# Kernel tuning notes

Hardware: AMD Instinct MI355X
Metric: run time of the kernel (lower is better)

Reference implementation:

```python
import jax, jax.numpy as jnp
import numpy as np

B, Q, K, D, H = 16, 128, 128, 512, 512
NEG = -1e6


def setup_inputs() -> dict:
    key = jax.random.key(0)
    ks = jax.random.split(key, 7)
    return {
        "queries": jax.random.normal(ks[0], (B, Q, D), dtype=jnp.float32),
        "keys": jax.random.normal(ks[1], (B, K, D), dtype=jnp.float32),
        "values": jax.random.normal(ks[2], (B, K, D), dtype=jnp.float32),
        "valid_lens": jax.random.randint(ks[3], (B,), 1, K + 1, dtype=jnp.int32),
        "Wq": jax.random.normal(ks[4], (D, H), dtype=jnp.float32) / np.sqrt(D),
        "Wk": jax.random.normal(ks[5], (D, H), dtype=jnp.float32) / np.sqrt(D),
        "wv": jax.random.normal(ks[6], (H,), dtype=jnp.float32) / np.sqrt(H),
    }


def reference(queries, keys, values, valid_lens, Wq, Wk, wv):
    # projections (LazyLinear, bias=False)
    q = jnp.einsum("bqd,dh->bqh", queries, Wq)  # [B,Q,H]
    k = jnp.einsum("bkd,dh->bkh", keys, Wk)    # [B,K,H]
    # broadcast add -> tanh -> reduce to scalar score (Bahdanau)
    feats = jnp.tanh(q[:, :, None, :] + k[:, None, :, :])  # [B,Q,K,H]
    scores = jnp.einsum("bqkh,h->bqk", feats, wv)           # [B,Q,K]
    # masked softmax over key dim using per-batch valid lengths
    mask = jnp.arange(scores.shape[-1])[None, None, :] < valid_lens[:, None, None]
    scores = jnp.where(mask, scores, NEG)
    attn = jax.nn.softmax(scores, axis=-1)                  # [B,Q,K]
    # dropout is identity in eval mode
    return jnp.einsum("bqk,bkv->bqv", attn, values)
```

## Files before the change

### kernel.cpp

```cpp
#include <hip/hip_runtime.h>

#define Bn 16
#define Qn 128
#define Kn 128
#define Dn 512
#define Hn 512
#define NEGV (-3.0e38f)
#define PSCALE 2.8853900817779268f

typedef short s16x8 __attribute__((ext_vector_type(8)));
typedef float f32x4 __attribute__((ext_vector_type(4)));

__device__ __forceinline__ float exp2_hw(float x) {
  float r;
  asm("v_exp_f32 %0, %1" : "=v"(r) : "v"(x));
  return r;
}
__device__ __forceinline__ float rcp_hw(float x) { return __builtin_amdgcn_rcpf(x); }
__device__ __forceinline__ unsigned short f2bf(float f) {
  unsigned int u = __float_as_uint(f);
  u += 0x7fff + ((u >> 16) & 1);
  return (unsigned short)(u >> 16);
}

__global__ __launch_bounds__(256) void convert_kernel(
    const float* __restrict__ queries, const float* __restrict__ keys,
    const float* __restrict__ Wq, const float* __restrict__ Wk,
    const float* __restrict__ values,
    unsigned short* __restrict__ Abf, unsigned short* __restrict__ Wt,
    unsigned short* __restrict__ Vt)
{
  const int bid = blockIdx.x, t = threadIdx.x;
  if (bid < 512) {
    const int gid = bid * 256 + t;
    const size_t base = (size_t)gid * 16;
    const float* src = (base < 1048576) ? (queries + base) : (keys + (base - 1048576));
    unsigned short o[16];
    #pragma unroll
    for (int j = 0; j < 4; ++j) {
      float4 v = *(const float4*)(src + j * 4);
      o[j * 4 + 0] = f2bf(v.x); o[j * 4 + 1] = f2bf(v.y);
      o[j * 4 + 2] = f2bf(v.z); o[j * 4 + 3] = f2bf(v.w);
    }
    #pragma unroll
    for (int j = 0; j < 4; ++j)
      *(ushort4*)(Abf + base + j * 4) = *(ushort4*)&o[j * 4];
  } else if (bid < 640) {
    const int tid = (bid - 512) * 256 + t;
    const int n = tid & 511, rest = tid >> 9;
    const int sel = rest >> 5, k16 = rest & 31;
    const float* W = sel ? Wk : Wq;
    unsigned short o[16];
    #pragma unroll
    for (int i = 0; i < 16; ++i)
      o[i] = f2bf(W[(size_t)(k16 * 16 + i) * Hn + n]);
    unsigned short* dst = Wt + (size_t)sel * 262144 + (size_t)n * 512 + k16 * 16;
    #pragma unroll
    for (int j = 0; j < 4; ++j) *(ushort4*)(dst + j * 4) = *(ushort4*)&o[j * 4];
  } else {
    const int tid = (bid - 640) * 256 + t;
    const int d = tid & 511, rest = tid >> 9;
    const int b = rest >> 2, k32 = rest & 3;
    unsigned short o[32];
    #pragma unroll
    for (int i = 0; i < 32; ++i)
      o[i] = f2bf(values[((size_t)(b * Kn + k32 * 32 + i)) * Dn + d]);
    unsigned short* dst = Vt + (size_t)b * 65536 + (size_t)d * 128 + k32 * 32;
    #pragma unroll
    for (int j = 0; j < 8; ++j) *(ushort4*)(dst + j * 4) = *(ushort4*)&o[j * 4];
  }
}

__global__ __launch_bounds__(256) void proj_mfma(
    const unsigned short* __restrict__ Abf, const unsigned short* __restrict__ Wt,
    const float* __restrict__ wv,
    float* __restrict__ QW, float* __restrict__ Ekq)
{
  __shared__ unsigned short Al[128][72];
  __shared__ unsigned short Bl[64][72];
  const int t = threadIdx.x, w = t >> 6, l = t & 63;
  const int wm = w >> 1, wn = w & 1;
  const int rowTile = blockIdx.x;
  const int n0 = blockIdx.y * 64;
  const int R0 = rowTile * 128;
  const bool isQ = rowTile < 16;
  const unsigned short* Wsel = Wt + (isQ ? 0 : 262144);

  f32x4 acc[4][2];
  #pragma unroll
  for (int m = 0; m < 4; ++m)
    #pragma unroll
    for (int n = 0; n < 2; ++n) acc[m][n] = (f32x4)0.f;

  const int lr = l & 15, lk = l >> 4;

  for (int k0 = 0; k0 < Hn; k0 += 64) {
    ushort4 ar[4][2], br[2][2];
    #pragma unroll
    for (int i = 0; i < 4; ++i) {
      int g = t + 256 * i, r = g >> 3, c = g & 7;
      const unsigned short* p = Abf + (size_t)(R0 + r) * Hn + k0 + c * 8;
      ar[i][0] = *(const ushort4*)p; ar[i][1] = *(const ushort4*)(p + 4);
    }
    #pragma unroll
    for (int i = 0; i < 2; ++i) {
      int g = t + 256 * i, r = g >> 3, c = g & 7;
      const unsigned short* p = Wsel + (size_t)(n0 + r) * Hn + k0 + c * 8;
      br[i][0] = *(const ushort4*)p; br[i][1] = *(const ushort4*)(p + 4);
    }
    __syncthreads();
    #pragma unroll
    for (int i = 0; i < 4; ++i) {
      int g = t + 256 * i, r = g >> 3, c = g & 7;
      *(ushort4*)&Al[r][c * 8] = ar[i][0]; *(ushort4*)&Al[r][c * 8 + 4] = ar[i][1];
    }
    #pragma unroll
    for (int i = 0; i < 2; ++i) {
      int g = t + 256 * i, r = g >> 3, c = g & 7;
      *(ushort4*)&Bl[r][c * 8] = br[i][0]; *(ushort4*)&Bl[r][c * 8 + 4] = br[i][1];
    }
    __syncthreads();
    #pragma unroll
    for (int ks = 0; ks < 2; ++ks) {
      s16x8 af[4], bf_[2];
      #pragma unroll
      for (int m = 0; m < 4; ++m)
        af[m] = *(const s16x8*)&Al[wm * 64 + m * 16 + lr][ks * 32 + lk * 8];
      #pragma unroll
      for (int n = 0; n < 2; ++n)
        bf_[n] = *(const s16x8*)&Bl[wn * 32 + n * 16 + lr][ks * 32 + lk * 8];
      #pragma unroll
      for (int m = 0; m < 4; ++m)
        #pragma unroll
        for (int n = 0; n < 2; ++n)
          acc[m][n] = __builtin_amdgcn_mfma_f32_16x16x32_bf16(af[m], bf_[n], acc[m][n], 0, 0, 0);
    }
    __syncthreads();
  }

  #pragma unroll
  for (int m = 0; m < 4; ++m)
    #pragma unroll
    for (int n = 0; n < 2; ++n)
      #pragma unroll
      for (int r = 0; r < 4; ++r) {
        int row = R0 + wm * 64 + m * 16 + lk * 4 + r;
        int col = n0 + wn * 32 + n * 16 + lr;
        float a = acc[m][n][r];
        if (isQ) {
          float F  = exp2_hw(-PSCALE * a);
          float WF = -2.f * wv[col] * F;
          float2 o = {WF, F};
          *(float2*)(QW + ((size_t)row * Hn + col) * 2) = o;
        } else {
          int krow = row - 2048;
          int bb = krow >> 7, k = krow & 127;
          Ekq[(size_t)bb * 65536 + (size_t)col * 128 + k] = exp2_hw(PSCALE * a);
        }
      }
}

__global__ __launch_bounds__(256) void score_kernel(
    const float* __restrict__ QW, const float* __restrict__ Ekq,
    float* __restrict__ Sp)
{
  const int id = blockIdx.x;
  const int g = id & 63, qt = id >> 6;
  const int b = g >> 2, hs = g & 3;
  const int t = threadIdx.x, w = t >> 6, l = t & 63;
  const int q  = qt * 16 + w * 4 + (l >> 4);
  const int k0 = (l & 15) * 8;
  const int h0 = hs * 128;

  const float* ek  = Ekq + (size_t)b * 65536 + (size_t)h0 * 128 + k0;
  const float* qwp = QW + ((size_t)(b * Qn + q) * Hn + h0) * 2;

  float acc[8];
  #pragma unroll
  for (int j = 0; j < 8; ++j) acc[j] = 0.f;

  float4 e0a = *(const float4*)(ek);
  float4 e0b = *(const float4*)(ek + 4);
  float4 e1a = *(const float4*)(ek + 128);
  float4 e1b = *(const float4*)(ek + 132);
  float4 qv  = *(const float4*)(qwp);

  #pragma unroll 2
  for (int hb = 0; hb < 64; ++hb) {
    float4 ce0a = e0a, ce0b = e0b, ce1a = e1a, ce1b = e1b, cqv = qv;
    if (hb < 63) {
      const float* ep = ek + (size_t)(2 * hb + 2) * 128;
      e0a = *(const float4*)(ep);
      e0b = *(const float4*)(ep + 4);
      e1a = *(const float4*)(ep + 128);
      e1b = *(const float4*)(ep + 132);
      qv  = *(const float4*)(qwp + hb * 4 + 4);
    }
    const float WF0 = cqv.x, F0 = cqv.y, WF1 = cqv.z, F1 = cqv.w;
    float d0, d1, num;
    d0 = F0 + ce0a.x; d1 = F1 + ce1a.x;
    num = __builtin_fmaf(WF0, d1, WF1 * d0);
    acc[0] = __builtin_fmaf(num, rcp_hw(d0 * d1), acc[0]);
    d0 = F0 + ce0a.y; d1 = F1 + ce1a.y;
    num = __builtin_fmaf(WF0, d1, WF1 * d0);
    acc[1] = __builtin_fmaf(num, rcp_hw(d0 * d1), acc[1]);
    d0 = F0 + ce0a.z; d1 = F1 + ce1a.z;
    num = __builtin_fmaf(WF0, d1, WF1 * d0);
    acc[2] = __builtin_fmaf(num, rcp_hw(d0 * d1), acc[2]);
    d0 = F0 + ce0a.w; d1 = F1 + ce1a.w;
    num = __builtin_fmaf(WF0, d1, WF1 * d0);
    acc[3] = __builtin_fmaf(num, rcp_hw(d0 * d1), acc[3]);
    d0 = F0 + ce0b.x; d1 = F1 + ce1b.x;
    num = __builtin_fmaf(WF0, d1, WF1 * d0);
    acc[4] = __builtin_fmaf(num, rcp_hw(d0 * d1), acc[4]);
    d0 = F0 + ce0b.y; d1 = F1 + ce1b.y;
    num = __builtin_fmaf(WF0, d1, WF1 * d0);
    acc[5] = __builtin_fmaf(num, rcp_hw(d0 * d1), acc[5]);
    d0 = F0 + ce0b.z; d1 = F1 + ce1b.z;
    num = __builtin_fmaf(WF0, d1, WF1 * d0);
    acc[6] = __builtin_fmaf(num, rcp_hw(d0 * d1), acc[6]);
    d0 = F0 + ce0b.w; d1 = F1 + ce1b.w;
    num = __builtin_fmaf(WF0, d1, WF1 * d0);
    acc[7] = __builtin_fmaf(num, rcp_hw(d0 * d1), acc[7]);
  }

  float4 o0 = {acc[0], acc[1], acc[2], acc[3]};
  float4 o1 = {acc[4], acc[5], acc[6], acc[7]};
  size_t sb = (((size_t)hs * Bn + b) * Qn + q) * Kn + k0;
  *(float4*)(Sp + sb) = o0;
  *(float4*)(Sp + sb + 4) = o1;
}

__global__ __launch_bounds__(512) void softmax_kernel(
    const float* __restrict__ Sp, const int* __restrict__ valid_lens,
    unsigned short* __restrict__ At)
{
  const int t = threadIdx.x;
  const int b = blockIdx.y;
  const int q = blockIdx.x * 16 + (t >> 5);
  const int k0 = (t & 31) * 4;
  const size_t base = ((size_t)b * Qn + q) * Kn + k0;

  float4 s0 = *(const float4*)(Sp + base);
  float4 s1 = *(const float4*)(Sp + base + 262144);
  float4 s2 = *(const float4*)(Sp + base + 524288);
  float4 s3 = *(const float4*)(Sp + base + 786432);
  float s[4] = {s0.x + s1.x + s2.x + s3.x, s0.y + s1.y + s2.y + s3.y,
                s0.z + s1.z + s2.z + s3.z, s0.w + s1.w + s2.w + s3.w};

  const int vlen = valid_lens[b];
  bool ok[4];
  float m = NEGV;
  #pragma unroll
  for (int j = 0; j < 4; ++j) {
    ok[j] = (k0 + j) < vlen;
    if (ok[j]) m = fmaxf(m, s[j]);
  }
  #pragma unroll
  for (int xm = 16; xm >= 1; xm >>= 1) m = fmaxf(m, __shfl_xor(m, xm, 32));
  float e[4], sum = 0.f;
  #pragma unroll
  for (int j = 0; j < 4; ++j) {
    e[j] = ok[j] ? exp2_hw((s[j] - m) * 1.44269504f) : 0.f;
    sum += e[j];
  }
  #pragma unroll
  for (int xm = 16; xm >= 1; xm >>= 1) sum += __shfl_xor(sum, xm, 32);
  float inv = rcp_hw(sum);
  ushort4 o = {f2bf(e[0] * inv), f2bf(e[1] * inv), f2bf(e[2] * inv), f2bf(e[3] * inv)};
  *(ushort4*)(At + base) = o;
}

__global__ __launch_bounds__(256) void av_mfma(
    const unsigned short* __restrict__ At, const unsigned short* __restrict__ Vt,
    float* __restrict__ out)
{
  __shared__ unsigned short AtL[128][72];
  __shared__ unsigned short VL[128][72];
  const int t = threadIdx.x, w = t >> 6, l = t & 63;
  const int wm = w >> 1, wn = w & 1;
  const int dt = blockIdx.x;
  const int b = blockIdx.y;
  const int lr = l & 15, lk = l >> 4;

  f32x4 acc[4][4];
  #pragma unroll
  for (int m = 0; m < 4; ++m)
    #pragma unroll
    for (int n = 0; n < 4; ++n) acc[m][n] = (f32x4)0.f;

  const unsigned short* Atb = At + (size_t)b * Qn * Kn;
  const unsigned short* Vtb = Vt + (size_t)b * 65536 + (size_t)dt * 128 * Kn;

  for (int k0 = 0; k0 < Kn; k0 += 64) {
    ushort4 ar[4][2], vr[4][2];
    #pragma unroll
    for (int i = 0; i < 4; ++i) {
      int g = t + 256 * i, r = g >> 3, c = g & 7;
      const unsigned short* p = Atb + (size_t)r * Kn + k0 + c * 8;
      ar[i][0] = *(const ushort4*)p; ar[i][1] = *(const ushort4*)(p + 4);
      const unsigned short* pv = Vtb + (size_t)r * Kn + k0 + c * 8;
      vr[i][0] = *(const ushort4*)pv; vr[i][1] = *(const ushort4*)(pv + 4);
    }
    __syncthreads();
    #pragma unroll
    for (int i = 0; i < 4; ++i) {
      int g = t + 256 * i, r = g >> 3, c = g & 7;
      *(ushort4*)&AtL[r][c * 8] = ar[i][0]; *(ushort4*)&AtL[r][c * 8 + 4] = ar[i][1];
      *(ushort4*)&VL[r][c * 8] = vr[i][0];  *(ushort4*)&VL[r][c * 8 + 4] = vr[i][1];
    }
    __syncthreads();
    #pragma unroll
    for (int ks = 0; ks < 2; ++ks) {
      s16x8 af[4], bf_[4];
      #pragma unroll
      for (int m = 0; m < 4; ++m)
        af[m] = *(const s16x8*)&AtL[wm * 64 + m * 16 + lr][ks * 32 + lk * 8];
      #pragma unroll
      for (int n = 0; n < 4; ++n)
        bf_[n] = *(const s16x8*)&VL[wn * 64 + n * 16 + lr][ks * 32 + lk * 8];
      #pragma unroll
      for (int m = 0; m < 4; ++m)
        #pragma unroll
        for (int n = 0; n < 4; ++n)
          acc[m][n] = __builtin_amdgcn_mfma_f32_16x16x32_bf16(af[m], bf_[n], acc[m][n], 0, 0, 0);
    }
    __syncthreads();
  }

  #pragma unroll
  for (int m = 0; m < 4; ++m)
    #pragma unroll
    for (int n = 0; n < 4; ++n)
      #pragma unroll
      for (int r = 0; r < 4; ++r) {
        int row = wm * 64 + m * 16 + lk * 4 + r;
        int col = dt * 128 + wn * 64 + n * 16 + lr;
        out[((size_t)(b * Qn) + row) * Dn + col] = acc[m][n][r];
      }
}

extern "C" void kernel_launch(void* const* d_in, const int* in_sizes, int n_in,
                              void* d_out, int out_size, void* d_ws, size_t ws_size,
                              hipStream_t stream) {
  const float* queries    = (const float*)d_in[0];
  const float* keys       = (const float*)d_in[1];
  const float* values     = (const float*)d_in[2];
  const int*   valid_lens = (const int*)d_in[3];
  const float* Wq         = (const float*)d_in[4];
  const float* Wk         = (const float*)d_in[5];
  const float* wv         = (const float*)d_in[6];
  float* out = (float*)d_out;

  unsigned short* Abf = (unsigned short*)d_ws;
  unsigned short* Wt  = Abf + 2097152;
  unsigned short* Vt  = Wt + 524288;
  float*          QW  = (float*)(Vt + 1048576);
  float*          Ekq = QW + 2097152;
  float*          Sp  = Ekq + 1048576;
  unsigned short* At  = (unsigned short*)(Sp + 1048576);

  convert_kernel<<<768, 256, 0, stream>>>(queries, keys, Wq, Wk, values, Abf, Wt, Vt);
  proj_mfma<<<dim3(32, 8), 256, 0, stream>>>(Abf, Wt, wv, QW, Ekq);
  score_kernel<<<512, 256, 0, stream>>>(QW, Ekq, Sp);
  softmax_kernel<<<dim3(8, 16), 512, 0, stream>>>(Sp, valid_lens, At);
  av_mfma<<<dim3(4, 16), 256, 0, stream>>>(At, Vt, out);
}
```

Baseline: 53.97 us.

## Split score H-reduction 8 ways, transpose Ek through LDS, restructure prefetch

The score kernel now splits the hidden dimension into 8 slices instead of 4 and launches twice as many blocks. This raises parallelism on the dominant elementwise stage, at the cost of twice the partial-score storage and softmax reads. The projection epilogue for keys now transposes the exp values through shared memory, so the Ekq writes become coalesced float4 stores instead of strided scalar stores. The score loop is also rewritten with two explicit register sets for double-buffered loads.

```diff
diff --git a/kernel.cpp b/kernel.cpp
--- a/kernel.cpp
+++ b/kernel.cpp
@@ -78,6 +78,7 @@
 {
   __shared__ unsigned short Al[128][72];
   __shared__ unsigned short Bl[64][72];
+  __shared__ float Tep[64][132];
   const int t = threadIdx.x, w = t >> 6, l = t & 63;
   const int wm = w >> 1, wn = w & 1;
   const int rowTile = blockIdx.x;
@@ -138,26 +139,81 @@
     __syncthreads();
   }
 
-  #pragma unroll
-  for (int m = 0; m < 4; ++m)
-    #pragma unroll
-    for (int n = 0; n < 2; ++n)
-      #pragma unroll
-      for (int r = 0; r < 4; ++r) {
-        int row = R0 + wm * 64 + m * 16 + lk * 4 + r;
-        int col = n0 + wn * 32 + n * 16 + lr;
-        float a = acc[m][n][r];
-        if (isQ) {
+  if (isQ) {
+    #pragma unroll
+    for (int m = 0; m < 4; ++m)
+      #pragma unroll
+      for (int n = 0; n < 2; ++n)
+        #pragma unroll
+        for (int r = 0; r < 4; ++r) {
+          int row = R0 + wm * 64 + m * 16 + lk * 4 + r;
+          int col = n0 + wn * 32 + n * 16 + lr;
+          float a = acc[m][n][r];
           float F  = exp2_hw(-PSCALE * a);
           float WF = -2.f * wv[col] * F;
           float2 o = {WF, F};
           *(float2*)(QW + ((size_t)row * Hn + col) * 2) = o;
-        } else {
-          int krow = row - 2048;
-          int bb = krow >> 7, k = krow & 127;
-          Ekq[(size_t)bb * 65536 + (size_t)col * 128 + k] = exp2_hw(PSCALE * a);
         }
-      }
+  } else {
+    const int bb = rowTile - 16;
+    #pragma unroll
+    for (int m = 0; m < 4; ++m)
+      #pragma unroll
+      for (int n = 0; n < 2; ++n)
+        #pragma unroll
+        for (int r = 0; r < 4; ++r) {
+          int row_l = wm * 64 + m * 16 + lk * 4 + r;
+          int col_l = wn * 32 + n * 16 + lr;
+          Tep[col_l][row_l] = exp2_hw(PSCALE * acc[m][n][r]);
+        }
+    __syncthreads();
+    const int hl = t >> 2, kq = (t & 3) * 32;
+    float* dst = Ekq + (size_t)bb * 65536 + (size_t)(n0 + hl) * 128 + kq;
+    #pragma unroll
+    for (int j = 0; j < 8; ++j)
+      *(float4*)(dst + j * 4) = *(const float4*)&Tep[hl][kq + j * 4];
+  }
+}
+
+struct ScoreSet { float4 e0a, e0b, e1a, e1b, qv; };
+
+__device__ __forceinline__ void load_set(ScoreSet& s, const float* ek,
+                                         const float* qwp, int hb) {
+  const float* ep = ek + (size_t)(2 * hb) * 128;
+  s.e0a = *(const float4*)(ep);
+  s.e0b = *(const float4*)(ep + 4);
+  s.e1a = *(const float4*)(ep + 128);
+  s.e1b = *(const float4*)(ep + 132);
+  s.qv  = *(const float4*)(qwp + 4 * hb);
+}
+
+__device__ __forceinline__ void compute_set(const ScoreSet& s, float acc[8]) {
+  const float WF0 = s.qv.x, F0 = s.qv.y, WF1 = s.qv.z, F1 = s.qv.w;
+  float d0, d1, num;
+  d0 = F0 + s.e0a.x; d1 = F1 + s.e1a.x;
+  num = __builtin_fmaf(WF0, d1, WF1 * d0);
+  acc[0] = __builtin_fmaf(num, rcp_hw(d0 * d1), acc[0]);
+  d0 = F0 + s.e0a.y; d1 = F1 + s.e1a.y;
+  num = __builtin_fmaf(WF0, d1, WF1 * d0);
+  acc[1] = __builtin_fmaf(num, rcp_hw(d0 * d1), acc[1]);
+  d0 = F0 + s.e0a.z; d1 = F1 + s.e1a.z;
+  num = __builtin_fmaf(WF0, d1, WF1 * d0);
+  acc[2] = __builtin_fmaf(num, rcp_hw(d0 * d1), acc[2]);
+  d0 = F0 + s.e0a.w; d1 = F1 + s.e1a.w;
+  num = __builtin_fmaf(WF0, d1, WF1 * d0);
+  acc[3] = __builtin_fmaf(num, rcp_hw(d0 * d1), acc[3]);
+  d0 = F0 + s.e0b.x; d1 = F1 + s.e1b.x;
+  num = __builtin_fmaf(WF0, d1, WF1 * d0);
+  acc[4] = __builtin_fmaf(num, rcp_hw(d0 * d1), acc[4]);
+  d0 = F0 + s.e0b.y; d1 = F1 + s.e1b.y;
+  num = __builtin_fmaf(WF0, d1, WF1 * d0);
+  acc[5] = __builtin_fmaf(num, rcp_hw(d0 * d1), acc[5]);
+  d0 = F0 + s.e0b.z; d1 = F1 + s.e1b.z;
+  num = __builtin_fmaf(WF0, d1, WF1 * d0);
+  acc[6] = __builtin_fmaf(num, rcp_hw(d0 * d1), acc[6]);
+  d0 = F0 + s.e0b.w; d1 = F1 + s.e1b.w;
+  num = __builtin_fmaf(WF0, d1, WF1 * d0);
+  acc[7] = __builtin_fmaf(num, rcp_hw(d0 * d1), acc[7]);
 }
 
 __global__ __launch_bounds__(256) void score_kernel(
@@ -165,12 +221,12 @@
     float* __restrict__ Sp)
 {
   const int id = blockIdx.x;
-  const int g = id & 63, qt = id >> 6;
-  const int b = g >> 2, hs = g & 3;
+  const int g = id & 127, qt = id >> 7;
+  const int b = g >> 3, hs = g & 7;
   const int t = threadIdx.x, w = t >> 6, l = t & 63;
   const int q  = qt * 16 + w * 4 + (l >> 4);
   const int k0 = (l & 15) * 8;
-  const int h0 = hs * 128;
+  const int h0 = hs * 64;
 
   const float* ek  = Ekq + (size_t)b * 65536 + (size_t)h0 * 128 + k0;
   const float* qwp = QW + ((size_t)(b * Qn + q) * Hn + h0) * 2;
@@ -179,49 +235,15 @@
   #pragma unroll
   for (int j = 0; j < 8; ++j) acc[j] = 0.f;
 
-  float4 e0a = *(const float4*)(ek);
-  float4 e0b = *(const float4*)(ek + 4);
-  float4 e1a = *(const float4*)(ek + 128);
-  float4 e1b = *(const float4*)(ek + 132);
-  float4 qv  = *(const float4*)(qwp);
-
-  #pragma unroll 2
-  for (int hb = 0; hb < 64; ++hb) {
-    float4 ce0a = e0a, ce0b = e0b, ce1a = e1a, ce1b = e1b, cqv = qv;
-    if (hb < 63) {
-      const float* ep = ek + (size_t)(2 * hb + 2) * 128;
-      e0a = *(const float4*)(ep);
-      e0b = *(const float4*)(ep + 4);
-      e1a = *(const float4*)(ep + 128);
-      e1b = *(const float4*)(ep + 132);
-      qv  = *(const float4*)(qwp + hb * 4 + 4);
-    }
-    const float WF0 = cqv.x, F0 = cqv.y, WF1 = cqv.z, F1 = cqv.w;
-    float d0, d1, num;
-    d0 = F0 + ce0a.x; d1 = F1 + ce1a.x;
-    num = __builtin_fmaf(WF0, d1, WF1 * d0);
-    acc[0] = __builtin_fmaf(num, rcp_hw(d0 * d1), acc[0]);
-    d0 = F0 + ce0a.y; d1 = F1 + ce1a.y;
-    num = __builtin_fmaf(WF0, d1, WF1 * d0);
-    acc[1] = __builtin_fmaf(num, rcp_hw(d0 * d1), acc[1]);
-    d0 = F0 + ce0a.z; d1 = F1 + ce1a.z;
-    num = __builtin_fmaf(WF0, d1, WF1 * d0);
-    acc[2] = __builtin_fmaf(num, rcp_hw(d0 * d1), acc[2]);
-    d0 = F0 + ce0a.w; d1 = F1 + ce1a.w;
-    num = __builtin_fmaf(WF0, d1, WF1 * d0);
-    acc[3] = __builtin_fmaf(num, rcp_hw(d0 * d1), acc[3]);
-    d0 = F0 + ce0b.x; d1 = F1 + ce1b.x;
-    num = __builtin_fmaf(WF0, d1, WF1 * d0);
-    acc[4] = __builtin_fmaf(num, rcp_hw(d0 * d1), acc[4]);
-    d0 = F0 + ce0b.y; d1 = F1 + ce1b.y;
-    num = __builtin_fmaf(WF0, d1, WF1 * d0);
-    acc[5] = __builtin_fmaf(num, rcp_hw(d0 * d1), acc[5]);
-    d0 = F0 + ce0b.z; d1 = F1 + ce1b.z;
-    num = __builtin_fmaf(WF0, d1, WF1 * d0);
-    acc[6] = __builtin_fmaf(num, rcp_hw(d0 * d1), acc[6]);
-    d0 = F0 + ce0b.w; d1 = F1 + ce1b.w;
-    num = __builtin_fmaf(WF0, d1, WF1 * d0);
-    acc[7] = __builtin_fmaf(num, rcp_hw(d0 * d1), acc[7]);
+  ScoreSet sA, sB;
+  load_set(sA, ek, qwp, 0);
+  load_set(sB, ek, qwp, 1);
+  #pragma unroll 4
+  for (int hb = 0; hb < 32; hb += 2) {
+    compute_set(sA, acc);
+    if (hb + 2 < 32) load_set(sA, ek, qwp, hb + 2);
+    compute_set(sB, acc);
+    if (hb + 3 < 32) load_set(sB, ek, qwp, hb + 3);
   }
 
   float4 o0 = {acc[0], acc[1], acc[2], acc[3]};
@@ -241,12 +263,12 @@
   const int k0 = (t & 31) * 4;
   const size_t base = ((size_t)b * Qn + q) * Kn + k0;
 
-  float4 s0 = *(const float4*)(Sp + base);
-  float4 s1 = *(const float4*)(Sp + base + 262144);
-  float4 s2 = *(const float4*)(Sp + base + 524288);
-  float4 s3 = *(const float4*)(Sp + base + 786432);
-  float s[4] = {s0.x + s1.x + s2.x + s3.x, s0.y + s1.y + s2.y + s3.y,
-                s0.z + s1.z + s2.z + s3.z, s0.w + s1.w + s2.w + s3.w};
+  float s[4] = {0.f, 0.f, 0.f, 0.f};
+  #pragma unroll
+  for (int p = 0; p < 8; ++p) {
+    float4 sv = *(const float4*)(Sp + base + (size_t)p * 262144);
+    s[0] += sv.x; s[1] += sv.y; s[2] += sv.z; s[3] += sv.w;
+  }
 
   const int vlen = valid_lens[b];
   bool ok[4];
@@ -358,11 +380,11 @@
   float*          QW  = (float*)(Vt + 1048576);
   float*          Ekq = QW + 2097152;
   float*          Sp  = Ekq + 1048576;
-  unsigned short* At  = (unsigned short*)(Sp + 1048576);
+  unsigned short* At  = (unsigned short*)(Sp + 2097152);
 
   convert_kernel<<<768, 256, 0, stream>>>(queries, keys, Wq, Wk, values, Abf, Wt, Vt);
   proj_mfma<<<dim3(32, 8), 256, 0, stream>>>(Abf, Wt, wv, QW, Ekq);
-  score_kernel<<<512, 256, 0, stream>>>(QW, Ekq, Sp);
+  score_kernel<<<1024, 256, 0, stream>>>(QW, Ekq, Sp);
   softmax_kernel<<<dim3(8, 16), 512, 0, stream>>>(Sp, valid_lens, At);
   av_mfma<<<dim3(4, 16), 256, 0, stream>>>(At, Vt, out);
 }
```

After: 54.93 us. No clear change (+1.8%).
